# Kernel optimization log

Measured on AMD Instinct MI355X. Metric: run time of the kernel, lower is better.

Reference implementation:

```python
import math
import jax, jax.numpy as jnp
import numpy as np

E = 1024
H = 16
D = E // H  # head_dim = 64
B, T = 4, 2048


def setup_inputs() -> dict:
    key = jax.random.key(0)
    ks = jax.random.split(key, 9)
    s = 1.0 / math.sqrt(E)
    inp = {
        "x": jax.random.normal(ks[0], (B, T, E), dtype=jnp.float32),
        "Wq": jax.random.uniform(ks[1], (E, E), jnp.float32, -s, s),
        "bq": jax.random.uniform(ks[2], (E,), jnp.float32, -s, s),
        "Wk": jax.random.uniform(ks[3], (E, E), jnp.float32, -s, s),
        "bk": jax.random.uniform(ks[4], (E,), jnp.float32, -s, s),
        "Wv": jax.random.uniform(ks[5], (E, E), jnp.float32, -s, s),
        "bv": jax.random.uniform(ks[6], (E,), jnp.float32, -s, s),
        "Wo": jax.random.uniform(ks[7], (E, E), jnp.float32, -s, s),
        "bo": jax.random.uniform(ks[8], (E,), jnp.float32, -s, s),
    }
    return inp


def reference(x, Wq, bq, Wk, bk, Wv, bv, Wo, bo):
    # Linear projections (torch Linear: y = x @ W.T + b)
    q = x @ Wq.T + bq
    k = x @ Wk.T + bk
    v = x @ Wv.T + bv
    # [B, T, E] -> [B, H, T, D]
    def split_heads(t):
        return t.reshape(B, T, H, D).transpose(0, 2, 1, 3)
    q, k, v = split_heads(q), split_heads(k), split_heads(v)
    # scaled dot-product attention; note scale uses head_dim (attention(self.head_dim))
    scores = jnp.einsum("bhqd,bhkd->bhqk", q, k) / math.sqrt(D)
    attn = jax.nn.softmax(scores, axis=-1)
    out = jnp.einsum("bhqk,bhkd->bhqd", attn, v)
    out = out.transpose(0, 2, 1, 3).reshape(B, T, E)
    return out @ Wo.T + bo
```

## Files before the change

kernel.cpp:

```cpp
#include <hip/hip_runtime.h>

typedef short bh8 __attribute__((ext_vector_type(8)));
typedef short bh4 __attribute__((ext_vector_type(4)));
typedef float f4 __attribute__((ext_vector_type(4)));
typedef unsigned int u32;
typedef u32 u32x2 __attribute__((ext_vector_type(2)));

#if __has_builtin(__builtin_amdgcn_exp2f)
#define EXP2(x) __builtin_amdgcn_exp2f(x)
#else
#define EXP2(x) exp2f(x)
#endif

__device__ __forceinline__ short f2bf(float f) {
  unsigned u = __float_as_uint(f);
  u += 0x7FFFu + ((u >> 16) & 1u);
  return (short)(u >> 16);
}

__device__ __forceinline__ void async16(const void* g, void* l) {
  __builtin_amdgcn_global_load_lds((const __attribute__((address_space(1))) void*)g,
                                   (__attribute__((address_space(3))) void*)l, 16, 0, 0);
}

__global__ void cvt_kernel(const float* __restrict__ in, short* __restrict__ out, int n4) {
  int i = blockIdx.x * blockDim.x + threadIdx.x;
  if (i < n4) {
    f4 v = *(const f4*)(in + (size_t)i * 4);
    bh4 o;
    o[0] = f2bf(v[0]); o[1] = f2bf(v[1]); o[2] = f2bf(v[2]); o[3] = f2bf(v[3]);
    *(bh4*)(out + (size_t)i * 4) = o;
  }
}

__global__ void cvt_w4(const float* __restrict__ w0, const float* __restrict__ w1,
                       const float* __restrict__ w2, const float* __restrict__ w3,
                       short* __restrict__ out, int n4_per) {
  const float* in = blockIdx.y == 0 ? w0 : blockIdx.y == 1 ? w1 : blockIdx.y == 2 ? w2 : w3;
  short* o = out + (size_t)blockIdx.y * (size_t)n4_per * 4;
  int i = blockIdx.x * blockDim.x + threadIdx.x;
  if (i < n4_per) {
    f4 v = *(const f4*)(in + (size_t)i * 4);
    bh4 q;
    q[0] = f2bf(v[0]); q[1] = f2bf(v[1]); q[2] = f2bf(v[2]); q[3] = f2bf(v[3]);
    *(bh4*)(o + (size_t)i * 4) = q;
  }
}

template <typename OutT, bool BROW>
__device__ __forceinline__ void gemm_body(const short* __restrict__ A, const short* __restrict__ Bw,
                                          const float* __restrict__ bias, OutT* __restrict__ C,
                                          int m0, int n0, int N, int K, float scale,
                                          short* a_lds, short* b_lds) {
  const int t = threadIdx.x;
  const int lane = t & 63, wave = t >> 6, quad = lane >> 4, l15 = lane & 15;
  const int mw = (wave >> 1) * 64, nw = (wave & 1) * 64;

  f4 acc[4][4];
#pragma unroll
  for (int i = 0; i < 4; ++i)
#pragma unroll
    for (int j = 0; j < 4; ++j) acc[i][j] = (f4){0.f, 0.f, 0.f, 0.f};

  for (int k0 = 0; k0 < K; k0 += 32) {
#pragma unroll
    for (int i = 0; i < 2; ++i) {
      int c = i * 256 + t;
      int m = c >> 2;
      int kq = (c & 3) ^ ((m >> 1) & 3);
      const short* ga = A + (size_t)(m0 + m) * K + k0 + kq * 8;
      const short* gb = Bw + (size_t)(n0 + m) * K + k0 + kq * 8;
      async16(ga, (char*)a_lds + (i * 256 + wave * 64) * 16);
      async16(gb, (char*)b_lds + (i * 256 + wave * 64) * 16);
    }
    __syncthreads();
    bh8 af[4], bfr[4];
#pragma unroll
    for (int ms = 0; ms < 4; ++ms) {
      int m = mw + ms * 16 + l15;
      int pos = m * 4 + (quad ^ ((m >> 1) & 3));
      af[ms] = *(const bh8*)(a_lds + pos * 8);
    }
#pragma unroll
    for (int ns = 0; ns < 4; ++ns) {
      int n = nw + ns * 16 + l15;
      int pos = n * 4 + (quad ^ ((n >> 1) & 3));
      bfr[ns] = *(const bh8*)(b_lds + pos * 8);
    }
#pragma unroll
    for (int ms = 0; ms < 4; ++ms)
#pragma unroll
      for (int ns = 0; ns < 4; ++ns)
        acc[ms][ns] = __builtin_amdgcn_mfma_f32_16x16x32_bf16(af[ms], bfr[ns], acc[ms][ns], 0, 0, 0);
    __syncthreads();
  }
#pragma unroll
  for (int ns = 0; ns < 4; ++ns) {
    int col = n0 + nw + ns * 16 + l15;
    float bcol = BROW ? 0.f : bias[col & 1023];
#pragma unroll
    for (int ms = 0; ms < 4; ++ms) {
      int row = m0 + mw + ms * 16 + quad * 4;
      float brow = BROW ? bias[row & 1023] : 0.f;
#pragma unroll
      for (int r = 0; r < 4; ++r) {
        float bv = BROW ? bias[(row + r) & 1023] : bcol;
        float v = (acc[ms][ns][r] + bv) * scale;
        if (sizeof(OutT) == 2)
          ((short*)C)[(size_t)(row + r) * N + col] = f2bf(v);
        else
          ((float*)C)[(size_t)(row + r) * N + col] = v;
      }
      (void)brow;
    }
  }
}

__global__ void gemm_qkv(const short* __restrict__ xb, const short* __restrict__ W3,
                         const float* __restrict__ bq, const float* __restrict__ bk,
                         const float* __restrict__ bv,
                         short* __restrict__ Qo, short* __restrict__ Ko, short* __restrict__ VTo,
                         float qscale) {
  __shared__ __align__(16) short a_lds[128 * 32];
  __shared__ __align__(16) short b_lds[128 * 32];
  const int which = blockIdx.x >> 3;
  if (which == 2) {
    const short* Wv = W3 + (size_t)2 * 1024 * 1024;
    gemm_body<short, true>(Wv, xb, bv, VTo, (blockIdx.x & 7) * 128, blockIdx.y * 128,
                           8192, 1024, 1.0f, a_lds, b_lds);
  } else {
    const short* Bw = W3 + (size_t)which * 1024 * 1024;
    const float* bias = which == 0 ? bq : bk;
    short* C = which == 0 ? Qo : Ko;
    float scale = which == 0 ? qscale : 1.0f;
    gemm_body<short, false>(xb, Bw, bias, C, blockIdx.y * 128, (blockIdx.x & 7) * 128,
                            1024, 1024, scale, a_lds, b_lds);
  }
}

__global__ void gemm_bt_f32(const short* __restrict__ A, const short* __restrict__ Bw,
                            const float* __restrict__ bias, float* __restrict__ C) {
  __shared__ __align__(16) short a_lds[128 * 32];
  __shared__ __align__(16) short b_lds[128 * 32];
  gemm_body<float, false>(A, Bw, bias, C, blockIdx.y * 128, blockIdx.x * 128, 1024, 1024, 1.0f,
                          a_lds, b_lds);
}

__global__ void attn_kernel(const short* __restrict__ Qb, const short* __restrict__ Kb,
                            const short* __restrict__ VTb, short* __restrict__ AO) {
  __shared__ __align__(16) short k_lds[64 * 64];
  __shared__ __align__(16) short vt_lds[64 * 64];
  __shared__ __align__(16) short p_lds[4][16 * 72];
  const int t = threadIdx.x, lane = t & 63, wave = t >> 6, quad = lane >> 4, l15 = lane & 15;
  const int bh = blockIdx.y, b = bh >> 4, h = bh & 15;
  const int q0 = blockIdx.x * 128;
  const size_t baseq = ((size_t)b * 2048) * 1024 + (size_t)h * 64;
  const size_t basev = ((size_t)h * 64) * 8192 + (size_t)b * 2048;

  bh8 qf[2][2];
#pragma unroll
  for (int mi = 0; mi < 2; ++mi)
#pragma unroll
    for (int ks = 0; ks < 2; ++ks)
      qf[mi][ks] = *(const bh8*)(Qb + baseq + (size_t)(q0 + wave * 32 + mi * 16 + l15) * 1024 + ks * 32 + quad * 8);

  f4 O[2][4];
  float l_part[2] = {0.f, 0.f};
#pragma unroll
  for (int mi = 0; mi < 2; ++mi)
#pragma unroll
    for (int di = 0; di < 4; ++di) O[mi][di] = (f4){0.f, 0.f, 0.f, 0.f};

  for (int kt = 0; kt < 2048; kt += 64) {
    __syncthreads();
#pragma unroll
    for (int i = 0; i < 2; ++i) {
      int c = i * 256 + t;
      int kk = c >> 3;
      int dq = (c & 7) ^ (kk & 7);
      async16(Kb + baseq + (size_t)(kt + kk) * 1024 + dq * 8,
              (char*)k_lds + (i * 256 + wave * 64) * 16);
    }
#pragma unroll
    for (int i = 0; i < 2; ++i) {
      int c = i * 256 + t;
      int d = c >> 3;
      int kc = (c & 7) ^ (d & 7);
      async16(VTb + basev + (size_t)d * 8192 + kt + kc * 8,
              (char*)vt_lds + (i * 256 + wave * 64) * 16);
    }
    __syncthreads();

    f4 ST[4][2];
#pragma unroll
    for (int mK = 0; mK < 4; ++mK) {
      int key = mK * 16 + l15;
      bh8 ka0 = *(const bh8*)(k_lds + (key * 8 + (quad ^ (key & 7))) * 8);
      bh8 ka1 = *(const bh8*)(k_lds + (key * 8 + ((quad + 4) ^ (key & 7))) * 8);
#pragma unroll
      for (int mi = 0; mi < 2; ++mi) {
        f4 s = (f4){-16.f, -16.f, -16.f, -16.f};
        s = __builtin_amdgcn_mfma_f32_16x16x32_bf16(ka0, qf[mi][0], s, 0, 0, 0);
        s = __builtin_amdgcn_mfma_f32_16x16x32_bf16(ka1, qf[mi][1], s, 0, 0, 0);
        ST[mK][mi] = s;
      }
    }

    bh8 pa[2][2];
#pragma unroll
    for (int mi = 0; mi < 2; ++mi) {
      float lp = 0.f;
#pragma unroll
      for (int mK = 0; mK < 4; ++mK) {
        float p0 = EXP2(ST[mK][mi][0]);
        float p1 = EXP2(ST[mK][mi][1]);
        float p2 = EXP2(ST[mK][mi][2]);
        float p3 = EXP2(ST[mK][mi][3]);
        lp += (p0 + p1) + (p2 + p3);
        u32 d0 = __builtin_amdgcn_perm(__float_as_uint(p1), __float_as_uint(p0), 0x07060302u);
        u32 d1 = __builtin_amdgcn_perm(__float_as_uint(p3), __float_as_uint(p2), 0x07060302u);
        u32x2 dd = {d0, d1};
        *(u32x2*)(&p_lds[wave][l15 * 72 + mK * 16 + quad * 4]) = dd;
      }
      l_part[mi] += lp;
#pragma unroll
      for (int ks = 0; ks < 2; ++ks)
        pa[mi][ks] = *(const bh8*)(&p_lds[wave][l15 * 72 + ks * 32 + quad * 8]);
    }

#pragma unroll
    for (int di = 0; di < 4; ++di) {
      int d = di * 16 + l15;
      bh8 vb0 = *(const bh8*)(vt_lds + (d * 8 + (quad ^ (d & 7))) * 8);
      bh8 vb1 = *(const bh8*)(vt_lds + (d * 8 + ((quad + 4) ^ (d & 7))) * 8);
#pragma unroll
      for (int mi = 0; mi < 2; ++mi) {
        f4 o = O[mi][di];
        o = __builtin_amdgcn_mfma_f32_16x16x32_bf16(pa[mi][0], vb0, o, 0, 0, 0);
        o = __builtin_amdgcn_mfma_f32_16x16x32_bf16(pa[mi][1], vb1, o, 0, 0, 0);
        O[mi][di] = o;
      }
    }
  }

#pragma unroll
  for (int mi = 0; mi < 2; ++mi) {
    float l0 = l_part[mi];
    l0 += __shfl_xor(l0, 16);
    l0 += __shfl_xor(l0, 32);
    float rl[4];
#pragma unroll
    for (int r = 0; r < 4; ++r) {
      float lb = __shfl(l0, quad * 4 + r);
      rl[r] = __builtin_amdgcn_rcpf(lb);
    }
#pragma unroll
    for (int di = 0; di < 4; ++di)
#pragma unroll
      for (int r = 0; r < 4; ++r) {
        int row = q0 + wave * 32 + mi * 16 + quad * 4 + r;
        AO[baseq + (size_t)row * 1024 + di * 16 + l15] = f2bf(O[mi][di][r] * rl[r]);
      }
  }
}

extern "C" void kernel_launch(void* const* d_in, const int* in_sizes, int n_in,
                              void* d_out, int out_size, void* d_ws, size_t ws_size,
                              hipStream_t stream) {
  const float* x  = (const float*)d_in[0];
  const float* Wq = (const float*)d_in[1];
  const float* bq = (const float*)d_in[2];
  const float* Wk = (const float*)d_in[3];
  const float* bk = (const float*)d_in[4];
  const float* Wv = (const float*)d_in[5];
  const float* bv = (const float*)d_in[6];
  const float* Wo = (const float*)d_in[7];
  const float* bo = (const float*)d_in[8];
  float* out = (float*)d_out;

  const int M = 8192, E = 1024;
  const size_t NX = (size_t)M * E;
  const size_t NW = (size_t)E * E;

  short* ws  = (short*)d_ws;
  short* xb  = ws;
  short* wqb = xb + NX;
  short* wob = wqb + 3 * NW;
  short* qb  = wob + NW;
  short* kb  = qb + NX;
  short* vt  = kb + NX;
  short* aob = xb;

  cvt_kernel<<<dim3((unsigned)(NX / 1024)), 256, 0, stream>>>(x, xb, (int)(NX / 4));
  cvt_w4<<<dim3((unsigned)(NW / 1024), 4), 256, 0, stream>>>(Wq, Wk, Wv, Wo, wqb, (int)(NW / 4));

  const float qscale = 0.18033688011112042f;
  gemm_qkv<<<dim3(24, 64), 256, 0, stream>>>(xb, wqb, bq, bk, bv, qb, kb, vt, qscale);

  attn_kernel<<<dim3(16, 64), 256, 0, stream>>>(qb, kb, vt, aob);

  gemm_bt_f32<<<dim3(8, 64), 256, 0, stream>>>(aob, wob, bo, out);
}
```

Before: 279.5 us.

## Split attention block across 8 waves with 16 query rows each

The attention kernel now runs 512 threads per block, and each wave owns 16 query rows instead of 32. This halves the per-wave Q fragments, accumulators and score registers, and each thread issues one async K/V load per tile instead of two. The goal is more waves in flight to hide LDS and global load latency. In exchange each K/V fragment read from LDS now feeds fewer MFMAs, so per-wave LDS traffic rises relative to compute and the larger block synchronises more waves.

```diff
diff --git a/kernel.cpp b/kernel.cpp
--- a/kernel.cpp
+++ b/kernel.cpp
@@ -146,106 +146,90 @@
                           a_lds, b_lds);
 }
 
-__global__ void attn_kernel(const short* __restrict__ Qb, const short* __restrict__ Kb,
-                            const short* __restrict__ VTb, short* __restrict__ AO) {
+__global__ __launch_bounds__(512, 8) void attn_kernel(const short* __restrict__ Qb,
+                                                      const short* __restrict__ Kb,
+                                                      const short* __restrict__ VTb,
+                                                      short* __restrict__ AO) {
   __shared__ __align__(16) short k_lds[64 * 64];
   __shared__ __align__(16) short vt_lds[64 * 64];
-  __shared__ __align__(16) short p_lds[4][16 * 72];
+  __shared__ __align__(16) short p_lds[8][16 * 72];
   const int t = threadIdx.x, lane = t & 63, wave = t >> 6, quad = lane >> 4, l15 = lane & 15;
   const int bh = blockIdx.y, b = bh >> 4, h = bh & 15;
   const int q0 = blockIdx.x * 128;
   const size_t baseq = ((size_t)b * 2048) * 1024 + (size_t)h * 64;
   const size_t basev = ((size_t)h * 64) * 8192 + (size_t)b * 2048;
 
-  bh8 qf[2][2];
-#pragma unroll
-  for (int mi = 0; mi < 2; ++mi)
-#pragma unroll
-    for (int ks = 0; ks < 2; ++ks)
-      qf[mi][ks] = *(const bh8*)(Qb + baseq + (size_t)(q0 + wave * 32 + mi * 16 + l15) * 1024 + ks * 32 + quad * 8);
-
-  f4 O[2][4];
-  float l_part[2] = {0.f, 0.f};
-#pragma unroll
-  for (int mi = 0; mi < 2; ++mi)
-#pragma unroll
-    for (int di = 0; di < 4; ++di) O[mi][di] = (f4){0.f, 0.f, 0.f, 0.f};
+  bh8 qf[2];
+#pragma unroll
+  for (int ks = 0; ks < 2; ++ks)
+    qf[ks] = *(const bh8*)(Qb + baseq + (size_t)(q0 + wave * 16 + l15) * 1024 + ks * 32 + quad * 8);
+
+  f4 O[4];
+  float l_part = 0.f;
+#pragma unroll
+  for (int di = 0; di < 4; ++di) O[di] = (f4){0.f, 0.f, 0.f, 0.f};
 
   for (int kt = 0; kt < 2048; kt += 64) {
     __syncthreads();
-#pragma unroll
-    for (int i = 0; i < 2; ++i) {
-      int c = i * 256 + t;
-      int kk = c >> 3;
-      int dq = (c & 7) ^ (kk & 7);
-      async16(Kb + baseq + (size_t)(kt + kk) * 1024 + dq * 8,
-              (char*)k_lds + (i * 256 + wave * 64) * 16);
-    }
-#pragma unroll
-    for (int i = 0; i < 2; ++i) {
-      int c = i * 256 + t;
-      int d = c >> 3;
-      int kc = (c & 7) ^ (d & 7);
-      async16(VTb + basev + (size_t)d * 8192 + kt + kc * 8,
-              (char*)vt_lds + (i * 256 + wave * 64) * 16);
-    }
-    __syncthreads();
-
-    f4 ST[4][2];
+    {
+      int kk = t >> 3;
+      int dq = (t & 7) ^ (kk & 7);
+      async16(Kb + baseq + (size_t)(kt + kk) * 1024 + dq * 8, (char*)k_lds + t * 16);
+    }
+    {
+      int d = t >> 3;
+      int kc = (t & 7) ^ (d & 7);
+      async16(VTb + basev + (size_t)d * 8192 + kt + kc * 8, (char*)vt_lds + t * 16);
+    }
+    __syncthreads();
+
+    f4 ST[4];
 #pragma unroll
     for (int mK = 0; mK < 4; ++mK) {
       int key = mK * 16 + l15;
       bh8 ka0 = *(const bh8*)(k_lds + (key * 8 + (quad ^ (key & 7))) * 8);
       bh8 ka1 = *(const bh8*)(k_lds + (key * 8 + ((quad + 4) ^ (key & 7))) * 8);
-#pragma unroll
-      for (int mi = 0; mi < 2; ++mi) {
-        f4 s = (f4){-16.f, -16.f, -16.f, -16.f};
-        s = __builtin_amdgcn_mfma_f32_16x16x32_bf16(ka0, qf[mi][0], s, 0, 0, 0);
-        s = __builtin_amdgcn_mfma_f32_16x16x32_bf16(ka1, qf[mi][1], s, 0, 0, 0);
-        ST[mK][mi] = s;
-      }
-    }
-
-    bh8 pa[2][2];
-#pragma unroll
-    for (int mi = 0; mi < 2; ++mi) {
+      f4 s = (f4){-16.f, -16.f, -16.f, -16.f};
+      s = __builtin_amdgcn_mfma_f32_16x16x32_bf16(ka0, qf[0], s, 0, 0, 0);
+      s = __builtin_amdgcn_mfma_f32_16x16x32_bf16(ka1, qf[1], s, 0, 0, 0);
+      ST[mK] = s;
+    }
+
+    {
       float lp = 0.f;
 #pragma unroll
       for (int mK = 0; mK < 4; ++mK) {
-        float p0 = EXP2(ST[mK][mi][0]);
-        float p1 = EXP2(ST[mK][mi][1]);
-        float p2 = EXP2(ST[mK][mi][2]);
-        float p3 = EXP2(ST[mK][mi][3]);
+        float p0 = EXP2(ST[mK][0]);
+        float p1 = EXP2(ST[mK][1]);
+        float p2 = EXP2(ST[mK][2]);
+        float p3 = EXP2(ST[mK][3]);
         lp += (p0 + p1) + (p2 + p3);
         u32 d0 = __builtin_amdgcn_perm(__float_as_uint(p1), __float_as_uint(p0), 0x07060302u);
         u32 d1 = __builtin_amdgcn_perm(__float_as_uint(p3), __float_as_uint(p2), 0x07060302u);
         u32x2 dd = {d0, d1};
         *(u32x2*)(&p_lds[wave][l15 * 72 + mK * 16 + quad * 4]) = dd;
       }
-      l_part[mi] += lp;
-#pragma unroll
-      for (int ks = 0; ks < 2; ++ks)
-        pa[mi][ks] = *(const bh8*)(&p_lds[wave][l15 * 72 + ks * 32 + quad * 8]);
-    }
-
+      l_part += lp;
+    }
+
+    bh8 pa[2];
+#pragma unroll
+    for (int ks = 0; ks < 2; ++ks)
+      pa[ks] = *(const bh8*)(&p_lds[wave][l15 * 72 + ks * 32 + quad * 8]);
 #pragma unroll
     for (int di = 0; di < 4; ++di) {
       int d = di * 16 + l15;
       bh8 vb0 = *(const bh8*)(vt_lds + (d * 8 + (quad ^ (d & 7))) * 8);
       bh8 vb1 = *(const bh8*)(vt_lds + (d * 8 + ((quad + 4) ^ (d & 7))) * 8);
-#pragma unroll
-      for (int mi = 0; mi < 2; ++mi) {
-        f4 o = O[mi][di];
-        o = __builtin_amdgcn_mfma_f32_16x16x32_bf16(pa[mi][0], vb0, o, 0, 0, 0);
-        o = __builtin_amdgcn_mfma_f32_16x16x32_bf16(pa[mi][1], vb1, o, 0, 0, 0);
-        O[mi][di] = o;
-      }
-    }
-  }
-
-#pragma unroll
-  for (int mi = 0; mi < 2; ++mi) {
-    float l0 = l_part[mi];
+      f4 o = O[di];
+      o = __builtin_amdgcn_mfma_f32_16x16x32_bf16(pa[0], vb0, o, 0, 0, 0);
+      o = __builtin_amdgcn_mfma_f32_16x16x32_bf16(pa[1], vb1, o, 0, 0, 0);
+      O[di] = o;
+    }
+  }
+
+  {
+    float l0 = l_part;
     l0 += __shfl_xor(l0, 16);
     l0 += __shfl_xor(l0, 32);
     float rl[4];
@@ -258,8 +242,8 @@
     for (int di = 0; di < 4; ++di)
 #pragma unroll
       for (int r = 0; r < 4; ++r) {
-        int row = q0 + wave * 32 + mi * 16 + quad * 4 + r;
-        AO[baseq + (size_t)row * 1024 + di * 16 + l15] = f2bf(O[mi][di][r] * rl[r]);
+        int row = q0 + wave * 16 + quad * 4 + r;
+        AO[baseq + (size_t)row * 1024 + di * 16 + l15] = f2bf(O[di][r] * rl[r]);
       }
   }
 }
@@ -297,7 +281,7 @@
   const float qscale = 0.18033688011112042f;
   gemm_qkv<<<dim3(24, 64), 256, 0, stream>>>(xb, wqb, bq, bk, bv, qb, kb, vt, qscale);
 
-  attn_kernel<<<dim3(16, 64), 256, 0, stream>>>(qb, kb, vt, aob);
+  attn_kernel<<<dim3(16, 64), 512, 0, stream>>>(qb, kb, vt, aob);
 
   gemm_bt_f32<<<dim3(8, 64), 256, 0, stream>>>(aob, wob, bo, out);
 }
```

Result: slower. 285.7 us (+2.2%).

## Use 2 waves per attention block, each handling 64 query rows

Applied to the files above, without the earlier changes.

The attention kernel now runs with 128 threads (2 waves) per block, and each wave processes 64 query rows instead of 32. K fragments are loaded from LDS once per tile and reused across four query sub-tiles, and V fragments are reused across four as well. This halves the LDS reads of K/V per query and the per-block async load traffic per wave pair, at the cost of higher register pressure (larger O accumulator and qf arrays) and fewer waves per block for latency hiding.

```diff
diff --git a/kernel.cpp b/kernel.cpp
--- a/kernel.cpp
+++ b/kernel.cpp
@@ -146,76 +146,77 @@
                           a_lds, b_lds);
 }
 
-__global__ void attn_kernel(const short* __restrict__ Qb, const short* __restrict__ Kb,
-                            const short* __restrict__ VTb, short* __restrict__ AO) {
+__global__ __launch_bounds__(128, 2) void attn_kernel(const short* __restrict__ Qb,
+                                                      const short* __restrict__ Kb,
+                                                      const short* __restrict__ VTb,
+                                                      short* __restrict__ AO) {
   __shared__ __align__(16) short k_lds[64 * 64];
   __shared__ __align__(16) short vt_lds[64 * 64];
-  __shared__ __align__(16) short p_lds[4][16 * 72];
+  __shared__ __align__(16) short p_lds[2][16 * 72];
   const int t = threadIdx.x, lane = t & 63, wave = t >> 6, quad = lane >> 4, l15 = lane & 15;
   const int bh = blockIdx.y, b = bh >> 4, h = bh & 15;
   const int q0 = blockIdx.x * 128;
   const size_t baseq = ((size_t)b * 2048) * 1024 + (size_t)h * 64;
   const size_t basev = ((size_t)h * 64) * 8192 + (size_t)b * 2048;
 
-  bh8 qf[2][2];
-#pragma unroll
-  for (int mi = 0; mi < 2; ++mi)
+  bh8 qf[4][2];
+#pragma unroll
+  for (int mi = 0; mi < 4; ++mi)
 #pragma unroll
     for (int ks = 0; ks < 2; ++ks)
-      qf[mi][ks] = *(const bh8*)(Qb + baseq + (size_t)(q0 + wave * 32 + mi * 16 + l15) * 1024 + ks * 32 + quad * 8);
-
-  f4 O[2][4];
-  float l_part[2] = {0.f, 0.f};
-#pragma unroll
-  for (int mi = 0; mi < 2; ++mi)
+      qf[mi][ks] = *(const bh8*)(Qb + baseq + (size_t)(q0 + wave * 64 + mi * 16 + l15) * 1024 + ks * 32 + quad * 8);
+
+  f4 O[4][4];
+  float l_part[4] = {0.f, 0.f, 0.f, 0.f};
+#pragma unroll
+  for (int mi = 0; mi < 4; ++mi)
 #pragma unroll
     for (int di = 0; di < 4; ++di) O[mi][di] = (f4){0.f, 0.f, 0.f, 0.f};
 
   for (int kt = 0; kt < 2048; kt += 64) {
     __syncthreads();
 #pragma unroll
-    for (int i = 0; i < 2; ++i) {
-      int c = i * 256 + t;
+    for (int i = 0; i < 4; ++i) {
+      int c = i * 128 + t;
       int kk = c >> 3;
       int dq = (c & 7) ^ (kk & 7);
-      async16(Kb + baseq + (size_t)(kt + kk) * 1024 + dq * 8,
-              (char*)k_lds + (i * 256 + wave * 64) * 16);
-    }
-#pragma unroll
-    for (int i = 0; i < 2; ++i) {
-      int c = i * 256 + t;
+      async16(Kb + baseq + (size_t)(kt + kk) * 1024 + dq * 8, (char*)k_lds + c * 16);
+    }
+#pragma unroll
+    for (int i = 0; i < 4; ++i) {
+      int c = i * 128 + t;
       int d = c >> 3;
       int kc = (c & 7) ^ (d & 7);
-      async16(VTb + basev + (size_t)d * 8192 + kt + kc * 8,
-              (char*)vt_lds + (i * 256 + wave * 64) * 16);
+      async16(VTb + basev + (size_t)d * 8192 + kt + kc * 8, (char*)vt_lds + c * 16);
     }
     __syncthreads();
 
-    f4 ST[4][2];
+    bh8 ka0[4], ka1[4];
 #pragma unroll
     for (int mK = 0; mK < 4; ++mK) {
       int key = mK * 16 + l15;
-      bh8 ka0 = *(const bh8*)(k_lds + (key * 8 + (quad ^ (key & 7))) * 8);
-      bh8 ka1 = *(const bh8*)(k_lds + (key * 8 + ((quad + 4) ^ (key & 7))) * 8);
-#pragma unroll
-      for (int mi = 0; mi < 2; ++mi) {
+      ka0[mK] = *(const bh8*)(k_lds + (key * 8 + (quad ^ (key & 7))) * 8);
+      ka1[mK] = *(const bh8*)(k_lds + (key * 8 + ((quad + 4) ^ (key & 7))) * 8);
+    }
+
+    bh8 pa[4][2];
+#pragma unroll
+    for (int mi = 0; mi < 4; ++mi) {
+      f4 ST[4];
+#pragma unroll
+      for (int mK = 0; mK < 4; ++mK) {
         f4 s = (f4){-16.f, -16.f, -16.f, -16.f};
-        s = __builtin_amdgcn_mfma_f32_16x16x32_bf16(ka0, qf[mi][0], s, 0, 0, 0);
-        s = __builtin_amdgcn_mfma_f32_16x16x32_bf16(ka1, qf[mi][1], s, 0, 0, 0);
-        ST[mK][mi] = s;
-      }
-    }
-
-    bh8 pa[2][2];
-#pragma unroll
-    for (int mi = 0; mi < 2; ++mi) {
+        s = __builtin_amdgcn_mfma_f32_16x16x32_bf16(ka0[mK], qf[mi][0], s, 0, 0, 0);
+        s = __builtin_amdgcn_mfma_f32_16x16x32_bf16(ka1[mK], qf[mi][1], s, 0, 0, 0);
+        ST[mK] = s;
+      }
       float lp = 0.f;
 #pragma unroll
       for (int mK = 0; mK < 4; ++mK) {
-        float p0 = EXP2(ST[mK][mi][0]);
-        float p1 = EXP2(ST[mK][mi][1]);
-        float p2 = EXP2(ST[mK][mi][2]);
-        float p3 = EXP2(ST[mK][mi][3]);
+        float p0 = EXP2(ST[mK][0]);
+        float p1 = EXP2(ST[mK][1]);
+        float p2 = EXP2(ST[mK][2]);
+        float p3 = EXP2(ST[mK][3]);
         lp += (p0 + p1) + (p2 + p3);
         u32 d0 = __builtin_amdgcn_perm(__float_as_uint(p1), __float_as_uint(p0), 0x07060302u);
         u32 d1 = __builtin_amdgcn_perm(__float_as_uint(p3), __float_as_uint(p2), 0x07060302u);
@@ -234,7 +235,7 @@
       bh8 vb0 = *(const bh8*)(vt_lds + (d * 8 + (quad ^ (d & 7))) * 8);
       bh8 vb1 = *(const bh8*)(vt_lds + (d * 8 + ((quad + 4) ^ (d & 7))) * 8);
 #pragma unroll
-      for (int mi = 0; mi < 2; ++mi) {
+      for (int mi = 0; mi < 4; ++mi) {
         f4 o = O[mi][di];
         o = __builtin_amdgcn_mfma_f32_16x16x32_bf16(pa[mi][0], vb0, o, 0, 0, 0);
         o = __builtin_amdgcn_mfma_f32_16x16x32_bf16(pa[mi][1], vb1, o, 0, 0, 0);
@@ -244,7 +245,7 @@
   }
 
 #pragma unroll
-  for (int mi = 0; mi < 2; ++mi) {
+  for (int mi = 0; mi < 4; ++mi) {
     float l0 = l_part[mi];
     l0 += __shfl_xor(l0, 16);
     l0 += __shfl_xor(l0, 32);
@@ -258,7 +259,7 @@
     for (int di = 0; di < 4; ++di)
 #pragma unroll
       for (int r = 0; r < 4; ++r) {
-        int row = q0 + wave * 32 + mi * 16 + quad * 4 + r;
+        int row = q0 + wave * 64 + mi * 16 + quad * 4 + r;
         AO[baseq + (size_t)row * 1024 + di * 16 + l15] = f2bf(O[mi][di][r] * rl[r]);
       }
   }
@@ -297,7 +298,7 @@
   const float qscale = 0.18033688011112042f;
   gemm_qkv<<<dim3(24, 64), 256, 0, stream>>>(xb, wqb, bq, bk, bv, qb, kb, vt, qscale);
 
-  attn_kernel<<<dim3(16, 64), 256, 0, stream>>>(qb, kb, vt, aob);
+  attn_kernel<<<dim3(16, 64), 128, 0, stream>>>(qb, kb, vt, aob);
 
   gemm_bt_f32<<<dim3(8, 64), 256, 0, stream>>>(aob, wob, bo, out);
 }
```

Result: no change. 282.5 us (+1.1%).

## Double-buffer LDS in GEMM body to overlap global loads with MFMA

Applied to the files above, without the earlier changes.

The shared GEMM routine now uses two LDS buffers. It issues the async global-to-LDS loads for the next K-slice before computing on the current one, and uses an explicit vmcnt wait plus barrier in place of two __syncthreads per iteration. It also raises wave priority around the MFMA block. This hides global load latency behind compute, at the cost of doubled LDS per block (32 KB), which may reduce occupancy. The attention kernel is unchanged, so only the QKV and output projections benefit.

```diff
diff --git a/kernel.cpp b/kernel.cpp
--- a/kernel.cpp
+++ b/kernel.cpp
@@ -62,7 +62,7 @@
 #pragma unroll
     for (int j = 0; j < 4; ++j) acc[i][j] = (f4){0.f, 0.f, 0.f, 0.f};
 
-  for (int k0 = 0; k0 < K; k0 += 32) {
+  auto stage = [&](int k0, int buf) {
 #pragma unroll
     for (int i = 0; i < 2; ++i) {
       int c = i * 256 + t;
@@ -70,29 +70,45 @@
       int kq = (c & 3) ^ ((m >> 1) & 3);
       const short* ga = A + (size_t)(m0 + m) * K + k0 + kq * 8;
       const short* gb = Bw + (size_t)(n0 + m) * K + k0 + kq * 8;
-      async16(ga, (char*)a_lds + (i * 256 + wave * 64) * 16);
-      async16(gb, (char*)b_lds + (i * 256 + wave * 64) * 16);
-    }
-    __syncthreads();
+      async16(ga, (char*)(a_lds + buf * 4096) + (i * 256 + wave * 64) * 16);
+      async16(gb, (char*)(b_lds + buf * 4096) + (i * 256 + wave * 64) * 16);
+    }
+  };
+
+  stage(0, 0);
+  asm volatile("s_waitcnt vmcnt(0)" ::: "memory");
+  __builtin_amdgcn_s_barrier();
+  asm volatile("" ::: "memory");
+
+  int cur = 0;
+  for (int k0 = 0; k0 < K; k0 += 32) {
+    if (k0 + 32 < K) stage(k0 + 32, cur ^ 1);
+    const short* al = a_lds + cur * 4096;
+    const short* bl = b_lds + cur * 4096;
     bh8 af[4], bfr[4];
 #pragma unroll
     for (int ms = 0; ms < 4; ++ms) {
       int m = mw + ms * 16 + l15;
       int pos = m * 4 + (quad ^ ((m >> 1) & 3));
-      af[ms] = *(const bh8*)(a_lds + pos * 8);
+      af[ms] = *(const bh8*)(al + pos * 8);
     }
 #pragma unroll
     for (int ns = 0; ns < 4; ++ns) {
       int n = nw + ns * 16 + l15;
       int pos = n * 4 + (quad ^ ((n >> 1) & 3));
-      bfr[ns] = *(const bh8*)(b_lds + pos * 8);
-    }
+      bfr[ns] = *(const bh8*)(bl + pos * 8);
+    }
+    __builtin_amdgcn_s_setprio(1);
 #pragma unroll
     for (int ms = 0; ms < 4; ++ms)
 #pragma unroll
       for (int ns = 0; ns < 4; ++ns)
         acc[ms][ns] = __builtin_amdgcn_mfma_f32_16x16x32_bf16(af[ms], bfr[ns], acc[ms][ns], 0, 0, 0);
-    __syncthreads();
+    __builtin_amdgcn_s_setprio(0);
+    asm volatile("s_waitcnt vmcnt(0)" ::: "memory");
+    __builtin_amdgcn_s_barrier();
+    asm volatile("" ::: "memory");
+    cur ^= 1;
   }
 #pragma unroll
   for (int ns = 0; ns < 4; ++ns) {
@@ -101,7 +117,6 @@
 #pragma unroll
     for (int ms = 0; ms < 4; ++ms) {
       int row = m0 + mw + ms * 16 + quad * 4;
-      float brow = BROW ? bias[row & 1023] : 0.f;
 #pragma unroll
       for (int r = 0; r < 4; ++r) {
         float bv = BROW ? bias[(row + r) & 1023] : bcol;
@@ -111,7 +126,6 @@
         else
           ((float*)C)[(size_t)(row + r) * N + col] = v;
       }
-      (void)brow;
     }
   }
 }
@@ -121,8 +135,8 @@
                          const float* __restrict__ bv,
                          short* __restrict__ Qo, short* __restrict__ Ko, short* __restrict__ VTo,
                          float qscale) {
-  __shared__ __align__(16) short a_lds[128 * 32];
-  __shared__ __align__(16) short b_lds[128 * 32];
+  __shared__ __align__(16) short a_lds[2 * 128 * 32];
+  __shared__ __align__(16) short b_lds[2 * 128 * 32];
   const int which = blockIdx.x >> 3;
   if (which == 2) {
     const short* Wv = W3 + (size_t)2 * 1024 * 1024;
@@ -140,8 +154,8 @@
 
 __global__ void gemm_bt_f32(const short* __restrict__ A, const short* __restrict__ Bw,
                             const float* __restrict__ bias, float* __restrict__ C) {
-  __shared__ __align__(16) short a_lds[128 * 32];
-  __shared__ __align__(16) short b_lds[128 * 32];
+  __shared__ __align__(16) short a_lds[2 * 128 * 32];
+  __shared__ __align__(16) short b_lds[2 * 128 * 32];
   gemm_body<float, false>(A, Bw, bias, C, blockIdx.y * 128, blockIdx.x * 128, 1024, 1024, 1.0f,
                           a_lds, b_lds);
 }
```

New measurement: 276.7 us. Within noise of the previous version (-1.0%).
